# Kernel tuning notes

Hardware: AMD Instinct MI355X
Metric: run time of the kernel (lower is better)

Reference implementation:

```python
import jax, jax.numpy as jnp
import numpy as np

DIM = 256      # block dim
NH = 4         # num_head
HD = DIM // 2  # head_dim = dim // 2 (per CrossBlock -> CroA)
HALF = DIM // 2  # channels per axial branch
DI = NH * HD   # inner qkv dim = 512
B, H, W = 8, 56, 56


def _conv1x1(w, b, x):
    # 1x1 conv == per-pixel channel matmul; w:[Cout,Cin], x:[B,Cin,H,W]
    return jnp.einsum('oc,bchw->bohw', w, x) + b[None, :, None, None]


def _mha(x, qw, qb, kw, kb, vw, vb, pw, pb, rel):
    # axial MHA over the last (W) axis, per row, matching torch MHA exactly
    Bx, C, Hx, Wx = x.shape
    q = _conv1x1(qw, qb, x).transpose(0, 2, 1, 3).reshape(Bx, Hx, NH, HD, Wx)
    k = _conv1x1(kw, kb, x).transpose(0, 2, 1, 3).reshape(Bx, Hx, NH, HD, Wx)
    v = _conv1x1(vw, vb, x).transpose(0, 2, 1, 3).reshape(Bx, Hx, NH, HD, Wx)
    att = jnp.einsum('bhndi,bhndj->bhnij', q, k) * (HD ** -0.5)
    L = Wx
    # gathered relative-position bias (RelPos); torch does this under no_grad
    idx = (jnp.arange(L)[:, None] - jnp.arange(L)[None, :] + L - 1).reshape(-1)
    bias = jax.lax.stop_gradient(rel[:, idx].reshape(NH, L, L))
    att = jax.nn.softmax(att + bias[None, None], axis=-1)
    out = jnp.einsum('bhnij,bhndj->bhnid', att, v)  # [B,H,nh,W,hd]
    # faithful to torch: raw reshape of [B*H, nh, W, hd] -> (B, H, W, nh*hd)
    out = out.reshape(Bx, Hx, Wx, NH * HD).transpose(0, 3, 1, 2)
    return _conv1x1(pw, pb, out) + x


def _forward(x, xq_w, xq_b, xk_w, xk_b, xv_w, xv_b, xp_w, xp_b, rel_x,
             yq_w, yq_b, yk_w, yk_b, yv_w, yv_b, yp_w, yp_b, rel_y,
             cp_w, cp_b, m1_w, m1_b, m2_w, m2_b, ls1, ls2):
    ax, ay = jnp.split(x, 2, axis=1)
    ax = _mha(ax, xq_w, xq_b, xk_w, xk_b, xv_w, xv_b, xp_w, xp_b, rel_x)
    ay = _mha(ay.transpose(0, 1, 3, 2), yq_w, yq_b, yk_w, yk_b, yv_w, yv_b,
              yp_w, yp_b, rel_y).transpose(0, 1, 3, 2)
    net = _conv1x1(cp_w, cp_b, jnp.concatenate([ax, ay], axis=1))
    net = net * ls1[None] + x                      # layer_scale1 + residual
    h = jax.nn.gelu(_conv1x1(m1_w, m1_b, net), approximate=False)
    out = _conv1x1(m2_w, m2_b, h)
    return out * ls2[None] + net                   # layer_scale2 + identity skip (dim==out_dim)


def setup_inputs() -> dict:
    key = jax.random.key(0)
    ks = iter(jax.random.split(key, 32))
    def w(shape, s=0.05):
        return jax.random.normal(next(ks), shape, dtype=jnp.float32) * s
    return dict(
        x=jax.random.normal(next(ks), (B, DIM, H, W), dtype=jnp.float32),
        xq_w=w((DI, HALF)), xq_b=w((DI,)), xk_w=w((DI, HALF)), xk_b=w((DI,)),
        xv_w=w((DI, HALF)), xv_b=w((DI,)), xp_w=w((HALF, DI)), xp_b=w((HALF,)),
        rel_x=jax.random.normal(next(ks), (NH, W * W), dtype=jnp.float32),
        yq_w=w((DI, HALF)), yq_b=w((DI,)), yk_w=w((DI, HALF)), yk_b=w((DI,)),
        yv_w=w((DI, HALF)), yv_b=w((DI,)), yp_w=w((HALF, DI)), yp_b=w((HALF,)),
        rel_y=jax.random.normal(next(ks), (NH, H * H), dtype=jnp.float32),
        cp_w=w((DIM, DIM)), cp_b=w((DIM,)),
        m1_w=w((2 * DIM, DIM)), m1_b=w((2 * DIM,)),
        m2_w=w((DIM, 2 * DIM)), m2_b=w((DIM,)),
        ls1=jnp.ones((DIM, 1, 1), jnp.float32),
        ls2=jnp.ones((DIM, 1, 1), jnp.float32),
    )


def reference(x, xq_w, xq_b, xk_w, xk_b, xv_w, xv_b, xp_w, xp_b, rel_x,
              yq_w, yq_b, yk_w, yk_b, yv_w, yv_b, yp_w, yp_b, rel_y,
              cp_w, cp_b, m1_w, m1_b, m2_w, m2_b, ls1, ls2):
    return _forward(x, xq_w, xq_b, xk_w, xk_b, xv_w, xv_b, xp_w, xp_b, rel_x,
                    yq_w, yq_b, yk_w, yk_b, yv_w, yv_b, yp_w, yp_b, rel_y,
                    cp_w, cp_b, m1_w, m1_b, m2_w, m2_b, ls1, ls2)
```

## Files before the change

kernel.cpp:

```cpp
#include <hip/hip_runtime.h>

using u16 = unsigned short;
using u32 = unsigned int;

typedef short bf16x8 __attribute__((ext_vector_type(8)));
typedef float f32x4 __attribute__((ext_vector_type(4)));

#define HW 3136
#define IMG 56

__device__ __forceinline__ float bf2f(u16 v) {
    union { u32 u; float f; } c; c.u = ((u32)v) << 16; return c.f;
}
__device__ __forceinline__ u16 f2bf(float f) {
    union { float f; u32 u; } c; c.f = f;
    return (u16)((c.u + 0x7fffu + ((c.u >> 16) & 1u)) >> 16);
}
__device__ __forceinline__ u32 pk2bf(float a, float b) {
    u32 r;
    asm("v_cvt_pk_bf16_f32 %0, %1, %2" : "=v"(r) : "v"(a), "v"(b));
    return r;
}
__device__ __forceinline__ int swz8(int r) { return (r ^ (r >> 3)) & 7; }

__device__ __forceinline__ f32x4 mfma16(bf16x8 a, bf16x8 b, f32x4 c) {
    return __builtin_amdgcn_mfma_f32_16x16x32_bf16(a, b, c, 0, 0, 0);
}

__device__ __forceinline__ void gl_lds(const void* g, void* l) {
    __builtin_amdgcn_global_load_lds((const __attribute__((address_space(1))) void*)g,
                                     (__attribute__((address_space(3))) void*)l, 16, 0, 0);
}

__global__ __launch_bounds__(256) void prep(
    const float* __restrict__ x, u16* __restrict__ Xt,
    const float* __restrict__ s0, const float* __restrict__ s1, const float* __restrict__ s2,
    const float* __restrict__ s3, const float* __restrict__ s4, const float* __restrict__ s5,
    const float* __restrict__ s6, const float* __restrict__ s7, const float* __restrict__ s8,
    const float* __restrict__ s9, const float* __restrict__ s10,
    const float* __restrict__ b0, const float* __restrict__ b1, const float* __restrict__ b2,
    const float* __restrict__ b3, const float* __restrict__ b4, const float* __restrict__ b5,
    const float* __restrict__ b6, const float* __restrict__ b7, const float* __restrict__ b8,
    const float* __restrict__ b9, const float* __restrict__ b10,
    u16* __restrict__ Wb, float* __restrict__ Bc)
{
    __shared__ u16 lds[64][80];
    const int t = threadIdx.x;
    const int idx = blockIdx.x;

    if (idx < 1568) {
        const int Pb = (idx % 49) * 64;
        const int Cb = ((idx / 49) & 3) * 64;
        const int b  = idx / 196;
        #pragma unroll
        for (int q = 0; q < 4; ++q) {
            int id = t + q * 256;
            int c = id >> 4, pf = (id & 15) * 4;
            float4 v = *(const float4*)(x + ((long)(b * 256 + Cb + c)) * HW + Pb + pf);
            u16 vv[4] = { f2bf(v.x), f2bf(v.y), f2bf(v.z), f2bf(v.w) };
            #pragma unroll
            for (int j = 0; j < 4; ++j) {
                int p = pf + j;
                int cc = (((c >> 3) ^ ((p >> 2) & 7)) << 3) + (c & 7);
                lds[p][cc] = vv[j];
            }
        }
        __syncthreads();
        int p = t >> 2, cf = (t & 3) * 16;
        u16* dst = Xt + ((long)b * HW + Pb + p) * 256 + Cb + cf;
        int cc0 = ((cf >> 3) + 0) ^ ((p >> 2) & 7);
        int cc1 = ((cf >> 3) + 1) ^ ((p >> 2) & 7);
        *(uint4*)(dst + 0) = *(uint4*)&lds[p][cc0 * 8];
        *(uint4*)(dst + 8) = *(uint4*)&lds[p][cc1 * 8];
        return;
    }

    const int bx = idx - 1568;
    if (bx == 832) {
        for (int i = t; i < 4352; i += 256) {
            const float* src; int off;
            if      (i < 512)  { src = b0;  off = i; }
            else if (i < 1024) { src = b1;  off = i - 512; }
            else if (i < 1536) { src = b2;  off = i - 1024; }
            else if (i < 2048) { src = b3;  off = i - 1536; }
            else if (i < 2560) { src = b4;  off = i - 2048; }
            else if (i < 3072) { src = b5;  off = i - 2560; }
            else if (i < 3200) { src = b6;  off = i - 3072; }
            else if (i < 3328) { src = b7;  off = i - 3200; }
            else if (i < 3584) { src = b8;  off = i - 3328; }
            else if (i < 4096) { src = b9;  off = i - 3584; }
            else               { src = b10; off = i - 4096; }
            Bc[i] = src[off];
        }
        return;
    }
    long gid4 = ((long)bx * 256 + t) * 4;
    const float* src; long off;
    if (gid4 < 589824) {
        int seg = (int)(gid4 >> 16);
        const float* tab[9] = { s0, s1, s2, s3, s4, s5, s6, s7, s8 };
        src = tab[seg]; off = gid4 - ((long)seg << 16);
    } else if (gid4 < 720896) { src = s9;  off = gid4 - 589824; }
    else                      { src = s10; off = gid4 - 720896; }
    float4 v = *(const float4*)(src + off);
    *(uint2*)(Wb + gid4) = make_uint2(pk2bf(v.x, v.y), pk2bf(v.z, v.w));
}

__global__ __launch_bounds__(256, 2) void fused_attn(
    const u16* __restrict__ Wb, const float* __restrict__ Bc,
    const u16* __restrict__ Xt,
    const float* __restrict__ rel_x, const float* __restrict__ rel_y,
    u16* __restrict__ SbX, u16* __restrict__ SbY)
{
    __shared__ __align__(16) char smem[66048];
    const int tid = threadIdx.x;
    const int lane = tid & 63, wid = tid >> 6;
    const int l15 = lane & 15, lg = lane >> 4;

    const int g = blockIdx.x;
    const int n = blockIdx.y;
    const int branch = blockIdx.z >> 3;
    const int b = blockIdx.z & 7;

    const float* rel = branch ? rel_y : rel_x;
    u16* S = branch ? SbY : SbX;
    const u16* wsrc = Wb + branch * 196608 + n * 16384;
    const float* bsrc = Bc + branch * 1536 + n * 128;

    if (tid < 128) {
        float v = (tid < 112) ? rel[n * HW + tid] : 0.0f;
        *(float*)(smem + 65536 + tid * 4) = v;
    }

    bf16x8 wf[3][2][4];
    #pragma unroll
    for (int mat = 0; mat < 3; ++mat)
        #pragma unroll
        for (int mt = 0; mt < 2; ++mt) {
            int mrow = (wid * 2 + mt) * 16 + l15;
            const u16* wr = wsrc + mat * 65536 + mrow * 128;
            #pragma unroll
            for (int ks = 0; ks < 4; ++ks)
                wf[mat][mt][ks] = *(const bf16x8*)(wr + (ks * 4 + lg) * 8);
        }
    float4 bq4[2], bk4[2]; float bvv[2];
    #pragma unroll
    for (int mt = 0; mt < 2; ++mt) {
        int m0 = (wid * 2 + mt) * 16 + lg * 4;
        bq4[mt] = *(const float4*)(bsrc + m0);
        bk4[mt] = *(const float4*)(bsrc + 512 + m0);
        bvv[mt] = bsrc[1024 + (wid * 2 + mt) * 16 + l15];
    }

    const int istrip = wid * 16;
    const float qscale = 0.08838834764831845f;

    auto stageX = [&](int rc2) {
        const int i0 = wid * 16 + (lane >> 4);
        #pragma unroll
        for (int t = 0; t < 4; ++t) {
            int i = i0 + t * 4;
            int ic = (i > 55) ? 55 : i;
            long p = (branch == 0) ? (long)rc2 * IMG + ic : (long)ic * IMG + rc2;
            const u16* src = Xt + ((long)b * HW + p) * 256 + branch * 128
                             + (((lane & 15) ^ swz8(i)) * 8);
            gl_lds(src, smem + 49152 + wid * 4096 + t * 1024);
        }
    };

    stageX(g * 7);

    for (int r = 0; r < 7; ++r) {
        const int rc = g * 7 + r;

        __syncthreads();

        bf16x8 xf[4][4];
        #pragma unroll
        for (int it = 0; it < 4; ++it) {
            int i = it * 16 + l15;
            #pragma unroll
            for (int ks = 0; ks < 4; ++ks)
                xf[it][ks] = *(const bf16x8*)(smem + 49152 + i * 256
                                              + (((ks * 4 + lg) ^ swz8(i)) * 16));
        }

        #pragma unroll
        for (int mat = 0; mat < 2; ++mat) {
            #pragma unroll
            for (int mt = 0; mt < 2; ++mt) {
                #pragma unroll
                for (int it = 0; it < 4; ++it) {
                    f32x4 a = {};
                    #pragma unroll
                    for (int ks = 0; ks < 4; ++ks)
                        a = mfma16(wf[mat][mt][ks], xf[it][ks], a);
                    int i = it * 16 + l15;
                    int m0 = (wid * 2 + mt) * 16 + lg * 4;
                    float4 bb2 = mat ? bk4[mt] : bq4[mt];
                    int c = m0 >> 3;
                    *(uint2*)(smem + mat * 16384 + i * 256 + ((c ^ swz8(i)) * 16) + (lg & 1) * 8)
                        = make_uint2(pk2bf(a[0] + bb2.x, a[1] + bb2.y),
                                     pk2bf(a[2] + bb2.z, a[3] + bb2.w));
                }
            }
        }
        #pragma unroll
        for (int mt = 0; mt < 2; ++mt) {
            #pragma unroll
            for (int it = 0; it < 4; ++it) {
                f32x4 a = {};
                #pragma unroll
                for (int ks = 0; ks < 4; ++ks)
                    a = mfma16(xf[it][ks], wf[2][mt][ks], a);
                int d = (wid * 2 + mt) * 16 + l15;
                int c2 = (it >> 1) * 4 + lg;
                float bv = bvv[mt];
                *(uint2*)(smem + 32768 + d * 128 + ((c2 ^ swz8(d)) * 16) + (it & 1) * 8)
                    = make_uint2(pk2bf(a[0] + bv, a[1] + bv),
                                 pk2bf(a[2] + bv, a[3] + bv));
            }
        }
        __syncthreads();

        if (r < 6) stageX(rc + 1);

        bf16x8 aq[4];
        #pragma unroll
        for (int ks = 0; ks < 4; ++ks) {
            int row = istrip + l15;
            int ch = ks * 4 + lg;
            aq[ks] = *(const bf16x8*)(smem + row * 256 + ((ch ^ swz8(row)) * 16));
        }
        f32x4 sacc[4] = {};
        #pragma unroll
        for (int ct = 0; ct < 4; ++ct) {
            #pragma unroll
            for (int ks = 0; ks < 4; ++ks) {
                int j = ct * 16 + l15;
                int ch = ks * 4 + lg;
                bf16x8 kb = *(const bf16x8*)(smem + 16384 + j * 256 + ((ch ^ swz8(j)) * 16));
                sacc[ct] = mfma16(kb, aq[ks], sacc[ct]);
            }
        }

        const int irow = istrip + l15;
        float p[4][4];
        float mx = -1e30f;
        #pragma unroll
        for (int ct = 0; ct < 4; ++ct)
            #pragma unroll
            for (int rr = 0; rr < 4; ++rr) {
                int j = ct * 16 + lg * 4 + rr;
                float x = sacc[ct][rr] * qscale;
                if (j < IMG) x += *(const float*)(smem + 65536 + (irow - j + 55) * 4);
                else x = -1e30f;
                p[ct][rr] = x;
                mx = fmaxf(mx, x);
            }
        mx = fmaxf(mx, __shfl_xor(mx, 16));
        mx = fmaxf(mx, __shfl_xor(mx, 32));
        float s0 = 0.f;
        #pragma unroll
        for (int ct = 0; ct < 4; ++ct)
            #pragma unroll
            for (int rr = 0; rr < 4; ++rr) {
                float e = __expf(p[ct][rr] - mx);
                p[ct][rr] = e; s0 += e;
            }
        s0 += __shfl_xor(s0, 16);
        s0 += __shfl_xor(s0, 32);
        float inv = 1.0f / s0;

        union { u32 u[4]; bf16x8 v; } pb[2];
        #pragma unroll
        for (int ks = 0; ks < 2; ++ks) {
            pb[ks].u[0] = pk2bf(p[2*ks][0] * inv, p[2*ks][1] * inv);
            pb[ks].u[1] = pk2bf(p[2*ks][2] * inv, p[2*ks][3] * inv);
            pb[ks].u[2] = pk2bf(p[2*ks+1][0] * inv, p[2*ks+1][1] * inv);
            pb[ks].u[3] = pk2bf(p[2*ks+1][2] * inv, p[2*ks+1][3] * inv);
        }

        f32x4 oacc[8] = {};
        #pragma unroll
        for (int dt = 0; dt < 8; ++dt) {
            #pragma unroll
            for (int ks = 0; ks < 2; ++ks) {
                int d = dt * 16 + l15;
                int c2 = ks * 4 + lg;
                bf16x8 vb = *(const bf16x8*)(smem + 32768 + d * 128 + ((c2 ^ swz8(d)) * 16));
                oacc[dt] = mfma16(vb, pb[ks].v, oacc[dt]);
            }
        }

        const int i = istrip + l15;
        if (i < IMG) {
            int im = n * 14 + (i >> 2);
            long pp = (branch == 0) ? (long)rc * IMG + im : (long)im * IMG + rc;
            u16* dst = S + ((long)b * HW + pp) * 512 + (i & 3) * 128;
            #pragma unroll
            for (int dt = 0; dt < 8; ++dt) {
                int d4 = dt * 16 + lg * 4;
                *(uint2*)(dst + d4) = make_uint2(pk2bf(oacc[dt][0], oacc[dt][1]),
                                                 pk2bf(oacc[dt][2], oacc[dt][3]));
            }
        }
    }
}

__global__ __launch_bounds__(256, 2) void tail(
    const u16* __restrict__ Wb, const float* __restrict__ Bc,
    const u16* __restrict__ SbX, const u16* __restrict__ SbY,
    const u16* __restrict__ Xt,
    const float* __restrict__ ls1, const float* __restrict__ ls2,
    u16* __restrict__ OUTp)
{
    __shared__ __align__(16) char smem[81920];
    const int tid = threadIdx.x;
    const int lane = tid & 63, wid = tid >> 6;
    const int l15 = lane & 15, lg = lane >> 4;
    const int P0 = blockIdx.x * 64;
    const int b  = blockIdx.z;

    const u16* xp  = Wb + 393216;
    const u16* yp  = Wb + 458752;
    const u16* cpw = Wb + 524288;
    const u16* m1w = Wb + 589824;
    const u16* m2w = Wb + 720896;

    f32x4 acc[4][4] = {};
    for (int ko = 0; ko < 512; ko += 64) {
        #pragma unroll
        for (int t = 0; t < 2; ++t) {
            int row = wid * 16 + t * 8 + (lane >> 3);
            int c = (lane & 7) ^ swz8(row);
            long prow = (long)b * HW + P0 + row;
            gl_lds(SbX + prow * 512 + ko + c * 8, smem + wid * 2048 + t * 1024);
            gl_lds(SbY + prow * 512 + ko + c * 8, smem + 8192 + wid * 2048 + t * 1024);
        }
        #pragma unroll
        for (int t = 0; t < 4; ++t) {
            int row = wid * 32 + t * 8 + (lane >> 3);
            int c = (lane & 7) ^ swz8(row);
            gl_lds(xp + (long)row * 512 + ko + c * 8, smem + 16384 + wid * 4096 + t * 1024);
            gl_lds(yp + (long)row * 512 + ko + c * 8, smem + 32768 + wid * 4096 + t * 1024);
        }
        __syncthreads();

        const int actb = (wid < 2) ? 0 : 8192;
        const int wbse = (wid < 2) ? 16384 : 32768;
        const int wrow0 = (wid & 1) * 64;
        #pragma unroll
        for (int ks = 0; ks < 2; ++ks) {
            int ch = ks * 4 + lg;
            bf16x8 af[4], bfr[4];
            #pragma unroll
            for (int rt = 0; rt < 4; ++rt) {
                int row = rt * 16 + l15;
                af[rt] = *(const bf16x8*)(smem + actb + row * 128 + ((ch ^ swz8(row)) * 16));
            }
            #pragma unroll
            for (int ct = 0; ct < 4; ++ct) {
                int row = wrow0 + ct * 16 + l15;
                bfr[ct] = *(const bf16x8*)(smem + wbse + row * 128 + ((ch ^ swz8(row)) * 16));
            }
            #pragma unroll
            for (int rt = 0; rt < 4; ++rt)
                #pragma unroll
                for (int ct = 0; ct < 4; ++ct)
                    acc[rt][ct] = mfma16(bfr[ct], af[rt], acc[rt][ct]);
        }
        __syncthreads();
    }

    #pragma unroll
    for (int rt = 0; rt < 4; ++rt) {
        int pl = rt * 16 + l15;
        long rowp = (long)b * HW + P0 + pl;
        #pragma unroll
        for (int ct = 0; ct < 4; ++ct) {
            int mg2 = wid * 64 + ct * 16 + lg * 4;
            float4 bv = *(const float4*)(Bc + 3072 + mg2);
            ushort4 rv = *(const ushort4*)(Xt + rowp * 256 + mg2);
            float v0 = acc[rt][ct][0] + bv.x + bf2f(rv.x);
            float v1 = acc[rt][ct][1] + bv.y + bf2f(rv.y);
            float v2 = acc[rt][ct][2] + bv.z + bf2f(rv.z);
            float v3 = acc[rt][ct][3] + bv.w + bf2f(rv.w);
            int cc = mg2 >> 3;
            int pos = (cc & 24) | ((cc ^ swz8(pl)) & 7);
            *(uint2*)(smem + 49152 + pl * 512 + pos * 16 + (mg2 & 7) * 2)
                = make_uint2(pk2bf(v0, v1), pk2bf(v2, v3));
        }
    }
    __syncthreads();

    f32x4 acc2[4][4] = {};
    for (int ko = 0; ko < 256; ko += 64) {
        #pragma unroll
        for (int t = 0; t < 8; ++t) {
            int row = wid * 64 + t * 8 + (lane >> 3);
            int c = (lane & 7) ^ swz8(row);
            gl_lds(cpw + (long)row * 256 + ko + c * 8, smem + 16384 + wid * 8192 + t * 1024);
        }
        __syncthreads();

        #pragma unroll
        for (int ks = 0; ks < 2; ++ks) {
            int ch = ks * 4 + lg;
            bf16x8 af[4], bfr[4];
            #pragma unroll
            for (int rt = 0; rt < 4; ++rt) {
                int row = rt * 16 + l15;
                int c = (ko >> 3) + ch;
                int pos = (c & 24) | ((c ^ swz8(row)) & 7);
                af[rt] = *(const bf16x8*)(smem + 49152 + row * 512 + pos * 16);
            }
            #pragma unroll
            for (int ct = 0; ct < 4; ++ct) {
                int row = wid * 64 + ct * 16 + l15;
                bfr[ct] = *(const bf16x8*)(smem + 16384 + row * 128 + ((ch ^ swz8(row)) * 16));
            }
            #pragma unroll
            for (int rt = 0; rt < 4; ++rt)
                #pragma unroll
                for (int ct = 0; ct < 4; ++ct)
                    acc2[rt][ct] = mfma16(bfr[ct], af[rt], acc2[rt][ct]);
        }
        __syncthreads();
    }

    #pragma unroll
    for (int rt = 0; rt < 4; ++rt) {
        int pl = rt * 16 + l15;
        long rowp = (long)b * HW + P0 + pl;
        #pragma unroll
        for (int ct = 0; ct < 4; ++ct) {
            int mg = wid * 64 + ct * 16 + lg * 4;
            float4 bv = *(const float4*)(Bc + 3328 + mg);
            float4 sv = *(const float4*)(ls1 + mg);
            ushort4 rv = *(const ushort4*)(Xt + rowp * 256 + mg);
            float v0 = (acc2[rt][ct][0] + bv.x) * sv.x + bf2f(rv.x);
            float v1 = (acc2[rt][ct][1] + bv.y) * sv.y + bf2f(rv.y);
            float v2 = (acc2[rt][ct][2] + bv.z) * sv.z + bf2f(rv.z);
            float v3 = (acc2[rt][ct][3] + bv.w) * sv.w + bf2f(rv.w);
            int cc = mg >> 3;
            int pos = (cc & 24) | ((cc ^ swz8(pl)) & 7);
            *(uint2*)(smem + 16384 + pl * 512 + pos * 16 + (mg & 7) * 2)
                = make_uint2(pk2bf(v0, v1), pk2bf(v2, v3));
        }
    }

    f32x4 aco[4][4] = {};

    for (int hc = 0; hc < 4; ++hc) {
        f32x4 ach[4][2] = {};
        for (int ko = 0; ko < 256; ko += 64) {
            #pragma unroll
            for (int t = 0; t < 4; ++t) {
                int row = wid * 32 + t * 8 + (lane >> 3);
                int c = (lane & 7) ^ swz8(row);
                gl_lds(m1w + (long)(hc * 128 + row) * 256 + ko + c * 8,
                       smem + wid * 4096 + t * 1024);
            }
            __syncthreads();

            #pragma unroll
            for (int ks = 0; ks < 2; ++ks) {
                int ch = ks * 4 + lg;
                bf16x8 af[4], bfrh[2];
                #pragma unroll
                for (int rt = 0; rt < 4; ++rt) {
                    int row = rt * 16 + l15;
                    int c = (ko >> 3) + ch;
                    int pos = (c & 24) | ((c ^ swz8(row)) & 7);
                    af[rt] = *(const bf16x8*)(smem + 16384 + row * 512 + pos * 16);
                }
                #pragma unroll
                for (int mt = 0; mt < 2; ++mt) {
                    int row = wid * 32 + mt * 16 + l15;
                    bfrh[mt] = *(const bf16x8*)(smem + row * 128 + ((ch ^ swz8(row)) * 16));
                }
                #pragma unroll
                for (int rt = 0; rt < 4; ++rt)
                    #pragma unroll
                    for (int mt = 0; mt < 2; ++mt)
                        ach[rt][mt] = mfma16(bfrh[mt], af[rt], ach[rt][mt]);
            }
            __syncthreads();
        }
        #pragma unroll
        for (int rt = 0; rt < 4; ++rt) {
            int pl = rt * 16 + l15;
            #pragma unroll
            for (int mt = 0; mt < 2; ++mt) {
                int hloc = wid * 32 + mt * 16 + lg * 4;
                float4 bv = *(const float4*)(Bc + 3584 + hc * 128 + hloc);
                float v[4];
                #pragma unroll
                for (int j = 0; j < 4; ++j) {
                    float tt = ach[rt][mt][j] + ((const float*)&bv)[j];
                    v[j] = tt * 0.5f * (1.0f + erff(tt * 0.70710678118f));
                }
                int cc = hloc >> 3;
                int pos = (cc & 8) | ((cc ^ swz8(pl)) & 7);
                *(uint2*)(smem + 49152 + pl * 256 + pos * 16 + (hloc & 7) * 2)
                    = make_uint2(pk2bf(v[0], v[1]), pk2bf(v[2], v[3]));
            }
        }

        for (int ko = 0; ko < 128; ko += 64) {
            #pragma unroll
            for (int t = 0; t < 8; ++t) {
                int row = wid * 64 + t * 8 + (lane >> 3);
                int c = (lane & 7) ^ swz8(row);
                char* dst = ((wid < 2) ? (smem + wid * 8192) : (smem + 65536 + (wid - 2) * 8192))
                            + t * 1024;
                gl_lds(m2w + (long)row * 512 + hc * 128 + ko + c * 8, dst);
            }
            __syncthreads();

            #pragma unroll
            for (int ks = 0; ks < 2; ++ks) {
                int ch = ks * 4 + lg;
                bf16x8 af[4], bfr[4];
                #pragma unroll
                for (int rt = 0; rt < 4; ++rt) {
                    int row = rt * 16 + l15;
                    int c = (ko >> 3) + ch;
                    int pos = (c & 8) | ((c ^ swz8(row)) & 7);
                    af[rt] = *(const bf16x8*)(smem + 49152 + row * 256 + pos * 16);
                }
                #pragma unroll
                for (int ct = 0; ct < 4; ++ct) {
                    int row = wid * 64 + ct * 16 + l15;
                    const char* base = (wid < 2) ? smem : (smem + 65536 - 16384);
                    bfr[ct] = *(const bf16x8*)(base + row * 128 + ((ch ^ swz8(row)) * 16));
                }
                #pragma unroll
                for (int rt = 0; rt < 4; ++rt)
                    #pragma unroll
                    for (int ct = 0; ct < 4; ++ct)
                        aco[rt][ct] = mfma16(bfr[ct], af[rt], aco[rt][ct]);
            }
            __syncthreads();
        }
    }

    #pragma unroll
    for (int rt = 0; rt < 4; ++rt) {
        int pl = rt * 16 + l15;
        long rowp = (long)b * HW + P0 + pl;
        #pragma unroll
        for (int ct = 0; ct < 4; ++ct) {
            int mg = wid * 64 + ct * 16 + lg * 4;
            float4 bv = *(const float4*)(Bc + 4096 + mg);
            float4 sv = *(const float4*)(ls2 + mg);
            int cc = mg >> 3;
            int pos = (cc & 24) | ((cc ^ swz8(pl)) & 7);
            uint2 nv2 = *(const uint2*)(smem + 16384 + pl * 512 + pos * 16 + (mg & 7) * 2);
            u16 nv[4] = { (u16)(nv2.x & 0xffff), (u16)(nv2.x >> 16),
                          (u16)(nv2.y & 0xffff), (u16)(nv2.y >> 16) };
            float v0 = (aco[rt][ct][0] + bv.x) * sv.x + bf2f(nv[0]);
            float v1 = (aco[rt][ct][1] + bv.y) * sv.y + bf2f(nv[1]);
            float v2 = (aco[rt][ct][2] + bv.z) * sv.z + bf2f(nv[2]);
            float v3 = (aco[rt][ct][3] + bv.w) * sv.w + bf2f(nv[3]);
            *(uint2*)(OUTp + rowp * 256 + mg) = make_uint2(pk2bf(v0, v1), pk2bf(v2, v3));
        }
    }
}

__global__ __launch_bounds__(256) void fuse_out(
    const u16* __restrict__ OUTp, float* __restrict__ y)
{
    __shared__ float lds[32][132];
    const int t = threadIdx.x;
    const int Pb = blockIdx.x * 128;
    const int Cb = blockIdx.y * 32;
    const int b  = blockIdx.z;

    #pragma unroll
    for (int q = 0; q < 4; ++q) {
        int id = t + q * 256;
        int p = id >> 3, cq = (id & 7) * 4;
        int pg = Pb + p;
        float4 v = make_float4(0.f, 0.f, 0.f, 0.f);
        if (pg < HW) {
            ushort4 nv = *(const ushort4*)(OUTp + ((long)b * HW + pg) * 256 + Cb + cq);
            v.x = bf2f(nv.x); v.y = bf2f(nv.y); v.z = bf2f(nv.z); v.w = bf2f(nv.w);
        }
        lds[cq + 0][p] = v.x; lds[cq + 1][p] = v.y;
        lds[cq + 2][p] = v.z; lds[cq + 3][p] = v.w;
    }
    __syncthreads();
    #pragma unroll
    for (int q = 0; q < 4; ++q) {
        int id = t + q * 256;
        int c = id >> 5, pq = (id & 31) * 4;
        int pg = Pb + pq;
        if (pg + 3 < HW) {
            float4 v = make_float4(lds[c][pq], lds[c][pq + 1], lds[c][pq + 2], lds[c][pq + 3]);
            *(float4*)(y + ((long)(b * 256 + Cb + c)) * HW + pg) = v;
        }
    }
}

extern "C" void kernel_launch(void* const* d_in, const int* in_sizes, int n_in,
                              void* d_out, int out_size, void* d_ws, size_t ws_size,
                              hipStream_t stream)
{
    const float* x     = (const float*)d_in[0];
    const float* xq_w  = (const float*)d_in[1];
    const float* xq_b  = (const float*)d_in[2];
    const float* xk_w  = (const float*)d_in[3];
    const float* xk_b  = (const float*)d_in[4];
    const float* xv_w  = (const float*)d_in[5];
    const float* xv_b  = (const float*)d_in[6];
    const float* xp_w  = (const float*)d_in[7];
    const float* xp_b  = (const float*)d_in[8];
    const float* rel_x = (const float*)d_in[9];
    const float* yq_w  = (const float*)d_in[10];
    const float* yq_b  = (const float*)d_in[11];
    const float* yk_w  = (const float*)d_in[12];
    const float* yk_b  = (const float*)d_in[13];
    const float* yv_w  = (const float*)d_in[14];
    const float* yv_b  = (const float*)d_in[15];
    const float* yp_w  = (const float*)d_in[16];
    const float* yp_b  = (const float*)d_in[17];
    const float* rel_y = (const float*)d_in[18];
    const float* cp_w  = (const float*)d_in[19];
    const float* cp_b  = (const float*)d_in[20];
    const float* m1_w  = (const float*)d_in[21];
    const float* m1_b  = (const float*)d_in[22];
    const float* m2_w  = (const float*)d_in[23];
    const float* m2_b  = (const float*)d_in[24];
    const float* ls1   = (const float*)d_in[25];
    const float* ls2   = (const float*)d_in[26];

    if (ws_size < 128450560) return;

    char* ws = (char*)d_ws;
    u16*   SbY  = (u16*)(ws + 0);
    u16*   OUTp = (u16*)(ws + 25690112);
    u16*   Xt   = (u16*)(ws + 77070336);
    u16*   SbX  = (u16*)(ws + 89915392);

    u16*   Wb = (u16*)d_out;
    float* Bc = (float*)((char*)d_out + 1703936);

    dim3 blk(256, 1, 1);

    prep<<<dim3(2401, 1, 1), blk, 0, stream>>>(
        x, Xt,
        xq_w, xk_w, xv_w, yq_w, yk_w, yv_w, xp_w, yp_w, cp_w, m1_w, m2_w,
        xq_b, xk_b, xv_b, yq_b, yk_b, yv_b, xp_b, yp_b, cp_b, m1_b, m2_b,
        Wb, Bc);
    fused_attn<<<dim3(8, 4, 16), blk, 0, stream>>>(Wb, Bc, Xt, rel_x, rel_y, SbX, SbY);
    tail<<<dim3(49, 1, 8), blk, 0, stream>>>(Wb, Bc, SbX, SbY, Xt, ls1, ls2, OUTp);
    fuse_out<<<dim3(25, 8, 8), blk, 0, stream>>>(OUTp, (float*)d_out);
}
```

Measured before the change: 136.5 us.

## Fuse NCHW fp32 output transpose into tail kernel and add MFMA priority hints

The tail kernel now transposes its results through shared memory and writes fp32 NCHW output directly, so the separate fuse_out kernel and the bf16 OUTp round trip are gone. Packed weights move from the output buffer into workspace because the output is now written while the weights are still being read. s_setprio raises wave priority around the MFMA sections in fused_attn to help overlap with other waves. This also removes an intermediate bf16 rounding of the output, at the cost of an extra LDS transpose stage in tail.

```diff
diff --git a/kernel.cpp b/kernel.cpp
--- a/kernel.cpp
+++ b/kernel.cpp
@@ -185,6 +185,7 @@
                                               + (((ks * 4 + lg) ^ swz8(i)) * 16));
         }
 
+        __builtin_amdgcn_s_setprio(1);
         #pragma unroll
         for (int mat = 0; mat < 2; ++mat) {
             #pragma unroll
@@ -221,6 +222,7 @@
                                  pk2bf(a[2] + bv, a[3] + bv));
             }
         }
+        __builtin_amdgcn_s_setprio(0);
         __syncthreads();
 
         if (r < 6) stageX(rc + 1);
@@ -232,6 +234,7 @@
             int ch = ks * 4 + lg;
             aq[ks] = *(const bf16x8*)(smem + row * 256 + ((ch ^ swz8(row)) * 16));
         }
+        __builtin_amdgcn_s_setprio(1);
         f32x4 sacc[4] = {};
         #pragma unroll
         for (int ct = 0; ct < 4; ++ct) {
@@ -243,6 +246,7 @@
                 sacc[ct] = mfma16(kb, aq[ks], sacc[ct]);
             }
         }
+        __builtin_amdgcn_s_setprio(0);
 
         const int irow = istrip + l15;
         float p[4][4];
@@ -281,6 +285,7 @@
             pb[ks].u[3] = pk2bf(p[2*ks+1][2] * inv, p[2*ks+1][3] * inv);
         }
 
+        __builtin_amdgcn_s_setprio(1);
         f32x4 oacc[8] = {};
         #pragma unroll
         for (int dt = 0; dt < 8; ++dt) {
@@ -292,6 +297,7 @@
                 oacc[dt] = mfma16(vb, pb[ks].v, oacc[dt]);
             }
         }
+        __builtin_amdgcn_s_setprio(0);
 
         const int i = istrip + l15;
         if (i < IMG) {
@@ -313,7 +319,7 @@
     const u16* __restrict__ SbX, const u16* __restrict__ SbY,
     const u16* __restrict__ Xt,
     const float* __restrict__ ls1, const float* __restrict__ ls2,
-    u16* __restrict__ OUTp)
+    float* __restrict__ y)
 {
     __shared__ __align__(16) char smem[81920];
     const int tid = threadIdx.x;
@@ -549,7 +555,6 @@
     #pragma unroll
     for (int rt = 0; rt < 4; ++rt) {
         int pl = rt * 16 + l15;
-        long rowp = (long)b * HW + P0 + pl;
         #pragma unroll
         for (int ct = 0; ct < 4; ++ct) {
             int mg = wid * 64 + ct * 16 + lg * 4;
@@ -560,47 +565,33 @@
             uint2 nv2 = *(const uint2*)(smem + 16384 + pl * 512 + pos * 16 + (mg & 7) * 2);
             u16 nv[4] = { (u16)(nv2.x & 0xffff), (u16)(nv2.x >> 16),
                           (u16)(nv2.y & 0xffff), (u16)(nv2.y >> 16) };
-            float v0 = (aco[rt][ct][0] + bv.x) * sv.x + bf2f(nv[0]);
-            float v1 = (aco[rt][ct][1] + bv.y) * sv.y + bf2f(nv[1]);
-            float v2 = (aco[rt][ct][2] + bv.z) * sv.z + bf2f(nv[2]);
-            float v3 = (aco[rt][ct][3] + bv.w) * sv.w + bf2f(nv[3]);
-            *(uint2*)(OUTp + rowp * 256 + mg) = make_uint2(pk2bf(v0, v1), pk2bf(v2, v3));
-        }
-    }
-}
-
-__global__ __launch_bounds__(256) void fuse_out(
-    const u16* __restrict__ OUTp, float* __restrict__ y)
-{
-    __shared__ float lds[32][132];
-    const int t = threadIdx.x;
-    const int Pb = blockIdx.x * 128;
-    const int Cb = blockIdx.y * 32;
-    const int b  = blockIdx.z;
+            aco[rt][ct][0] = (aco[rt][ct][0] + bv.x) * sv.x + bf2f(nv[0]);
+            aco[rt][ct][1] = (aco[rt][ct][1] + bv.y) * sv.y + bf2f(nv[1]);
+            aco[rt][ct][2] = (aco[rt][ct][2] + bv.z) * sv.z + bf2f(nv[2]);
+            aco[rt][ct][3] = (aco[rt][ct][3] + bv.w) * sv.w + bf2f(nv[3]);
+        }
+    }
+    __syncthreads();
 
     #pragma unroll
-    for (int q = 0; q < 4; ++q) {
-        int id = t + q * 256;
-        int p = id >> 3, cq = (id & 7) * 4;
-        int pg = Pb + p;
-        float4 v = make_float4(0.f, 0.f, 0.f, 0.f);
-        if (pg < HW) {
-            ushort4 nv = *(const ushort4*)(OUTp + ((long)b * HW + pg) * 256 + Cb + cq);
-            v.x = bf2f(nv.x); v.y = bf2f(nv.y); v.z = bf2f(nv.z); v.w = bf2f(nv.w);
-        }
-        lds[cq + 0][p] = v.x; lds[cq + 1][p] = v.y;
-        lds[cq + 2][p] = v.z; lds[cq + 3][p] = v.w;
+    for (int rt = 0; rt < 4; ++rt) {
+        int pl = rt * 16 + l15;
+        #pragma unroll
+        for (int ct = 0; ct < 4; ++ct) {
+            int mg = wid * 64 + ct * 16 + lg * 4;
+            #pragma unroll
+            for (int j = 0; j < 4; ++j)
+                ((float*)smem)[(mg + j) * 65 + pl] = aco[rt][ct][j];
+        }
     }
     __syncthreads();
-    #pragma unroll
-    for (int q = 0; q < 4; ++q) {
-        int id = t + q * 256;
-        int c = id >> 5, pq = (id & 31) * 4;
-        int pg = Pb + pq;
-        if (pg + 3 < HW) {
-            float4 v = make_float4(lds[c][pq], lds[c][pq + 1], lds[c][pq + 2], lds[c][pq + 3]);
-            *(float4*)(y + ((long)(b * 256 + Cb + c)) * HW + pg) = v;
-        }
+
+    {
+        const float* srcr = (const float*)smem + tid * 65;
+        float* dst = y + ((long)(b * 256 + tid)) * HW + P0;
+        #pragma unroll
+        for (int k = 0; k < 16; ++k)
+            *(float4*)(dst + k * 4) = *(const float4*)(srcr + k * 4);
     }
 }
 
@@ -640,12 +631,10 @@
 
     char* ws = (char*)d_ws;
     u16*   SbY  = (u16*)(ws + 0);
-    u16*   OUTp = (u16*)(ws + 25690112);
+    u16*   Wb   = (u16*)(ws + 25690112);
+    float* Bc   = (float*)(ws + 27394048);
     u16*   Xt   = (u16*)(ws + 77070336);
     u16*   SbX  = (u16*)(ws + 89915392);
-
-    u16*   Wb = (u16*)d_out;
-    float* Bc = (float*)((char*)d_out + 1703936);
 
     dim3 blk(256, 1, 1);
 
@@ -655,6 +644,5 @@
         xq_b, xk_b, xv_b, yq_b, yk_b, yv_b, xp_b, yp_b, cp_b, m1_b, m2_b,
         Wb, Bc);
     fused_attn<<<dim3(8, 4, 16), blk, 0, stream>>>(Wb, Bc, Xt, rel_x, rel_y, SbX, SbY);
-    tail<<<dim3(49, 1, 8), blk, 0, stream>>>(Wb, Bc, SbX, SbY, Xt, ls1, ls2, OUTp);
-    fuse_out<<<dim3(25, 8, 8), blk, 0, stream>>>(OUTp, (float*)d_out);
-}
+    tail<<<dim3(49, 1, 8), blk, 0, stream>>>(Wb, Bc, SbX, SbY, Xt, ls1, ls2, (float*)d_out);
+}
```

Result: faster. 132.7 us (-2.8%).
